# Kernel optimization log

Measured on AMD Instinct MI355X. Metric: run time of the kernel, lower is better.

## Reference

```python
import jax, jax.numpy as jnp
import numpy as np


def lstm_cell(x, h, c, Wih, Whh, b):
    # PyTorch LSTM gate order: i, f, g, o
    z = x @ Wih.T + h @ Whh.T + b
    i, f, g, o = jnp.split(z, 4, axis=-1)
    c = jax.nn.sigmoid(f) * c + jax.nn.sigmoid(i) * jnp.tanh(g)
    h = jax.nn.sigmoid(o) * jnp.tanh(c)
    return h, c


def run_dir(xs, Wih, Whh, b, reverse):
    # xs: [S, B, D_in] -> outputs [S, B, H], final (h, c)
    B = xs.shape[1]
    H = Whh.shape[1]
    init = (jnp.zeros((B, H), xs.dtype), jnp.zeros((B, H), xs.dtype))
    def step(carry, x):
        h, c = carry
        h, c = lstm_cell(x, h, c, Wih, Whh, b)
        return (h, c), h
    (h, c), ys = jax.lax.scan(step, init, xs, reverse=reverse)
    return ys, h, c


def _p(k, shape, scale=0.05):
    return jax.random.normal(k, shape, dtype=jnp.float32) * scale


def setup_inputs():
    V, E, H = 32000, 128, 256
    B, S, T = 32, 256, 64
    ks = jax.random.split(jax.random.key(0), 24)
    return {
        "src": jax.random.randint(ks[0], (B, S), 0, V),
        "tgt": jax.random.randint(ks[1], (B, T), 0, V),
        "emb": _p(ks[2], (V, E), 1.0),
        "enc_Wih_l0": _p(ks[3], (2, 4 * H, E)),
        "enc_Whh_l0": _p(ks[4], (2, 4 * H, H)),
        "enc_b_l0": _p(ks[5], (2, 4 * H)),
        "enc_Wih_l1": _p(ks[6], (2, 4 * H, 2 * H)),
        "enc_Whh_l1": _p(ks[7], (2, 4 * H, H)),
        "enc_b_l1": _p(ks[8], (2, 4 * H)),
        "dec_Wih0": _p(ks[9], (8 * H, E + 2 * H)),
        "dec_Whh0": _p(ks[10], (8 * H, 2 * H)),
        "dec_b0": _p(ks[11], (8 * H,)),
        "dec_Wih1": _p(ks[12], (8 * H, 2 * H)),
        "dec_Whh1": _p(ks[13], (8 * H, 2 * H)),
        "dec_b1": _p(ks[14], (8 * H,)),
        "attn_W1": _p(ks[15], (H, 4 * H)),
        "attn_b1": _p(ks[16], (H,)),
        "attn_W2": _p(ks[17], (1, H)),
        "attn_b2": _p(ks[18], (1,)),
        "out_W1": _p(ks[19], (H, 2 * H)),
        "out_b1": _p(ks[20], (H,)),
        "out_W2": _p(ks[21], (V, H)),
        "out_b2": _p(ks[22], (V,)),
    }


def reference(src, tgt, emb, enc_Wih_l0, enc_Whh_l0, enc_b_l0, enc_Wih_l1, enc_Whh_l1, enc_b_l1, dec_Wih0, dec_Whh0, dec_b0, dec_Wih1, dec_Whh1, dec_b1, attn_W1, attn_b1, attn_W2, attn_b2, out_W1, out_b1, out_W2, out_b2):
    # dropout layers are identity in eval mode
    H2 = dec_Whh0.shape[1]  # 2*hidden_dim = 512
    src_e = emb[src]                        # [B, S, E]
    tgt_e = emb[tgt]                        # [B, T, E]
    xs = jnp.swapaxes(src_e, 0, 1)          # [S, B, E]

    # 2-layer bidirectional encoder
    yf, hf0, cf0 = run_dir(xs, enc_Wih_l0[0], enc_Whh_l0[0], enc_b_l0[0], False)
    yb, hb0, cb0 = run_dir(xs, enc_Wih_l0[1], enc_Whh_l0[1], enc_b_l0[1], True)
    y0 = jnp.concatenate([yf, yb], axis=-1)  # [S, B, 2H]
    yf1, hf1, cf1 = run_dir(y0, enc_Wih_l1[0], enc_Whh_l1[0], enc_b_l1[0], False)
    yb1, hb1, cb1 = run_dir(y0, enc_Wih_l1[1], enc_Whh_l1[1], enc_b_l1[1], True)
    enc_out = jnp.swapaxes(jnp.concatenate([yf1, yb1], axis=-1), 0, 1)  # [B, S, 2H]

    # decoder init: per-layer concat of fwd/bwd final states (matches the view/transpose)
    h0 = jnp.concatenate([hf0, hb0], axis=-1)
    c0 = jnp.concatenate([cf0, cb0], axis=-1)
    h1 = jnp.concatenate([hf1, hb1], axis=-1)
    c1 = jnp.concatenate([cf1, cb1], axis=-1)

    # attention: Linear(4H, H) split into decoder-hidden part and encoder part
    W1_dec = attn_W1[:, :H2]
    W1_enc = attn_W1[:, H2:]
    enc_proj = jnp.einsum('bsd,hd->bsh', enc_out, W1_enc) + attn_b1  # precompute once

    dec_xs = jnp.swapaxes(tgt_e[:, :-1, :], 0, 1)  # [T-1, B, E]

    def step(carry, x_t):
        h0, c0, h1, c1 = carry
        e = jnp.tanh(enc_proj + (h1 @ W1_dec.T)[:, None, :])  # [B, S, H]
        scores = e @ attn_W2[0] + attn_b2[0]                  # [B, S]
        a = jax.nn.softmax(scores, axis=1)
        ctx = jnp.einsum('bs,bsd->bd', a, enc_out)            # [B, 2H]
        x = jnp.concatenate([x_t, ctx], axis=-1)              # [B, E+2H]
        h0, c0 = lstm_cell(x, h0, c0, dec_Wih0, dec_Whh0, dec_b0)
        h1, c1 = lstm_cell(h0, h1, c1, dec_Wih1, dec_Whh1, dec_b1)
        hid = jax.nn.relu(h1 @ out_W1.T + out_b1)
        logits = hid @ out_W2.T + out_b2                      # [B, V]
        return (h0, c0, h1, c1), logits

    _, ys = jax.lax.scan(step, (h0, c0, h1, c1), dec_xs)      # [T-1, B, V]
    return jnp.swapaxes(ys, 0, 1)                             # [B, T-1, V]
```

## Files before the change

kernel.cpp:

```cpp
#include <hip/hip_runtime.h>

#define BB_ 32
#define SS_ 256
#define TD_ 63
#define EE_ 128
#define VV_ 32000

typedef unsigned short u16;
typedef unsigned int u32;
typedef unsigned long long u64;
typedef __attribute__((ext_vector_type(8))) short short8v;
typedef __attribute__((ext_vector_type(4))) float f32x4;

__device__ __forceinline__ float sigf(float x){ return 1.0f/(1.0f+__expf(-x)); }
__device__ __forceinline__ float tanhf_fast(float x){ return 1.0f - 2.0f/(__expf(2.0f*x)+1.0f); }
__device__ __forceinline__ u16 f2bf(float f){
  unsigned u = __float_as_uint(f);
  u += 0x7fff + ((u >> 16) & 1);
  return (u16)(u >> 16);
}
__device__ __forceinline__ u32 packbf(float a, float b){
  return (u32)f2bf(a) | ((u32)f2bf(b) << 16);
}
__device__ __forceinline__ float bflo(u32 v){ return __uint_as_float(v << 16); }
__device__ __forceinline__ float bfhi(u32 v){ return __uint_as_float(v & 0xffff0000u); }

__device__ __forceinline__ u32 aldu(const u32* p){
  return __hip_atomic_load(p, __ATOMIC_RELAXED, __HIP_MEMORY_SCOPE_AGENT);
}
__device__ __forceinline__ u64 ald64u(const u32* p){
  return __hip_atomic_load((const u64*)p, __ATOMIC_RELAXED, __HIP_MEMORY_SCOPE_AGENT);
}
__device__ __forceinline__ void astu(u32* p, u32 v){
  __hip_atomic_store(p, v, __ATOMIC_RELAXED, __HIP_MEMORY_SCOPE_AGENT);
}
__device__ __forceinline__ float aldf(const float* p){
  return __hip_atomic_load(p, __ATOMIC_RELAXED, __HIP_MEMORY_SCOPE_AGENT);
}
__device__ __forceinline__ void astf(float* p, float v){
  __hip_atomic_store(p, v, __ATOMIC_RELAXED, __HIP_MEMORY_SCOPE_AGENT);
}
__device__ __forceinline__ void vdrain(){ asm volatile("s_waitcnt vmcnt(0)" ::: "memory"); }

__device__ __forceinline__ short8v mkfrag(u64 a, u64 b){
  union { u32 u[4]; short8v v; } c;
  c.u[0] = (u32)a; c.u[1] = (u32)(a >> 32);
  c.u[2] = (u32)b; c.u[3] = (u32)(b >> 32);
  return c.v;
}

__device__ __forceinline__ f32x4 mma8(const char* ldsA, int akk0, const u32* brow,
                                      int boff, int lk, int l, f32x4 acc){
  u64 bq[16];
  #pragma unroll
  for (int k2 = 0; k2 < 8; k2++){
    int a = boff + k2*16 + lk*4;
    bq[2*k2]   = ald64u(brow + a);
    bq[2*k2+1] = ald64u(brow + a + 2);
  }
  #pragma unroll
  for (int k2 = 0; k2 < 8; k2++){
    short8v aF = *(const short8v*)(ldsA + (((akk0 + k2)*64) + l)*16);
    acc = __builtin_amdgcn_mfma_f32_16x16x32_bf16(aF, mkfrag(bq[2*k2], bq[2*k2+1]), acc, 0, 0, 0);
  }
  return acc;
}

#define OFF_Z        0u
#define OFF_Y0       16777216u
#define OFF_Y1       20971520u
#define OFF_ZPRE     25165824u
#define OFF_H1ALL    29294592u
#define OFF_SRCE     30326784u
#define OFF_TGTE     31375360u
#define OFF_EPROJ    31633408u
#define OFF_ENCA0    33730560u
#define OFF_ENCA1    33992704u
#define OFF_DECA     34254848u
#define OFF_ATP      36352000u
#define OFF_E0H      36417536u
#define OFF_E0C      36433920u
#define OFF_E1H      36450304u
#define OFF_E1C      36466688u
#define OFF_H0P      36483072u
#define OFF_H1P      36499456u
#define OFF_CTXP     36515840u
#define OFF_CTXS     36532224u
#define OFF_Y1P      36532288u
#define OFF_HEXA     38629440u
#define OFF_HEXB     38645824u
#define OFF_BARS     38662208u

__device__ __forceinline__ void icbar(unsigned* ctr, unsigned target){
  vdrain();
  __syncthreads();
  if (threadIdx.x == 0){
    __hip_atomic_fetch_add(ctr, 1u, __ATOMIC_RELAXED, __HIP_MEMORY_SCOPE_AGENT);
    while (__hip_atomic_load(ctr, __ATOMIC_RELAXED, __HIP_MEMORY_SCOPE_AGENT) < target)
      __builtin_amdgcn_s_sleep(2);
  }
  __syncthreads();
  asm volatile("" ::: "memory");
}

__device__ __forceinline__ void icbar2(unsigned* base, unsigned gen){
  vdrain();
  __syncthreads();
  if (threadIdx.x == 0){
    unsigned g = blockIdx.x & 15u;
    unsigned old = __hip_atomic_fetch_add(&base[g*16], 1u, __ATOMIC_RELAXED, __HIP_MEMORY_SCOPE_AGENT);
    if ((old & 7u) == 7u)
      __hip_atomic_fetch_add(&base[256], 1u, __ATOMIC_RELAXED, __HIP_MEMORY_SCOPE_AGENT);
    while (__hip_atomic_load(&base[256], __ATOMIC_RELAXED, __HIP_MEMORY_SCOPE_AGENT) < gen*16u)
      __builtin_amdgcn_s_sleep(2);
  }
  __syncthreads();
  asm volatile("" ::: "memory");
}

__global__ void k_zero(float* __restrict__ p, int n){
  int i = blockIdx.x*256 + threadIdx.x;
  if (i < n) p[i] = 0.f;
}

__global__ void k_gather(const int* __restrict__ src, const int* __restrict__ tgt,
                         const float* __restrict__ emb,
                         float* __restrict__ src_e, float* __restrict__ tgt_e){
  int idx = blockIdx.x*256 + threadIdx.x;
  const int total = (8192 + 2016) * 32;
  if (idx >= total) return;
  int row = idx >> 5, j = idx & 31;
  int tok; float* dst;
  if (row < 8192){
    int s = row >> 5, b = row & 31;
    tok = src[b*SS_ + s];
    dst = src_e + (size_t)row*EE_;
  } else {
    int r2 = row - 8192;
    int t = r2 >> 5, b = r2 & 31;
    tok = tgt[b*64 + t];
    dst = tgt_e + (size_t)r2*EE_;
  }
  float4 v = *(const float4*)(emb + (size_t)tok*EE_ + j*4);
  *(float4*)(dst + j*4) = v;
}

__global__ void k_prep_encA(const float* __restrict__ W, u16* __restrict__ out){
  int idx = blockIdx.x*256 + threadIdx.x;
  if (idx >= 524288) return;
  int j = idx & 7, l = (idx>>3)&63, kk = (idx>>9)&7, m = (idx>>12)&7, us = (idx>>15)&7, d = (idx>>18)&1;
  int r = l & 15, g = r & 3, ut = r >> 2;
  int gcol = g*256 + us*32 + m*4 + ut;
  int k = kk*32 + (l>>4)*8 + j;
  out[idx] = f2bf(W[((size_t)d*1024 + gcol)*256 + k]);
}

__global__ void k_prep_decA(const float* __restrict__ Wih0, const float* __restrict__ Whh0,
                            const float* __restrict__ Wih1, const float* __restrict__ Whh1,
                            u16* __restrict__ out){
  int idx = blockIdx.x*256 + threadIdx.x;
  if (idx >= 4194304) return;
  int j = idx & 7, l = (idx>>3)&63, kk = (idx>>9)&31, cell = (idx>>14)&1, B = idx>>15;
  int r = l & 15;
  int ul = r >> 2, g = r & 3;
  int gcol = g*512 + B*4 + ul;
  int k = kk*32 + (l>>4)*8 + j;
  float wv;
  if (cell == 0) wv = (k < 512) ? Wih0[(size_t)gcol*640 + 128 + k] : Whh0[(size_t)gcol*512 + k - 512];
  else           wv = (k < 512) ? Wih1[(size_t)gcol*512 + k]       : Whh1[(size_t)gcol*512 + k - 512];
  out[idx] = f2bf(wv);
}

__global__ void k_prep_aTp(const float* __restrict__ aW1, u32* __restrict__ aTp){
  int idx = blockIdx.x*256 + threadIdx.x;
  if (idx >= 65536) return;
  int j2 = idx >> 8, c = idx & 255;
  aTp[idx] = packbf(aW1[(size_t)c*1024 + 2*j2], aW1[(size_t)c*1024 + 2*j2 + 1]);
}

__global__ void k_dinit(const float* __restrict__ eh0, const float* __restrict__ eh1,
                        u32* __restrict__ h0p, u32* __restrict__ h1p){
  int idx = blockIdx.x*256 + threadIdx.x;
  if (idx >= 8192) return;
  int b = idx >> 8, i = idx & 255;
  int dd = (2*i) >> 8, uu = (2*i) & 255;
  const float* p0 = eh0 + ((size_t)dd*32 + b)*256 + uu;
  const float* p1 = eh1 + ((size_t)dd*32 + b)*256 + uu;
  h0p[b*256 + i] = packbf(p0[0], p0[1]);
  h1p[b*256 + i] = packbf(p1[0], p1[1]);
}

__global__ __launch_bounds__(256) void k_mgemm(
    const float* __restrict__ A, const float* __restrict__ Bm,
    const float* __restrict__ bias, float* __restrict__ C,
    int M, int N, int K, int ldb, int boff, int flags){
  __shared__ u16 As[128*72];
  __shared__ u16 Bs[128*72];
  int tid = threadIdx.x;
  int m0 = blockIdx.x*128, n0 = blockIdx.y*128;
  int l = tid & 63, w = tid >> 6;
  int wr = w >> 1, wc = w & 1;
  int lr = l & 15, lk = (l >> 4) * 8;
  f32x4 acc[4][4];
  #pragma unroll
  for (int m=0;m<4;m++)
    #pragma unroll
    for (int n=0;n<4;n++) acc[m][n] = (f32x4){0.f,0.f,0.f,0.f};

  int r = tid >> 1, half = tid & 1;
  bool aval = (m0 + r) < M;
  const float* arow = A + (size_t)(m0 + r)*K + half*32;
  const float* brow = Bm + (size_t)(n0 + r)*ldb + boff + half*32;
  u16* asd = &As[r*72 + half*32];
  u16* bsd = &Bs[r*72 + half*32];

  for (int k0 = 0; k0 < K; k0 += 64){
    #pragma unroll
    for (int j = 0; j < 4; j++){
      float4 x = make_float4(0.f,0.f,0.f,0.f), y = x;
      if (aval){
        x = *(const float4*)(arow + k0 + j*8);
        y = *(const float4*)(arow + k0 + j*8 + 4);
      }
      asd[j*8+0]=f2bf(x.x); asd[j*8+1]=f2bf(x.y); asd[j*8+2]=f2bf(x.z); asd[j*8+3]=f2bf(x.w);
      asd[j*8+4]=f2bf(y.x); asd[j*8+5]=f2bf(y.y); asd[j*8+6]=f2bf(y.z); asd[j*8+7]=f2bf(y.w);
      float4 p = *(const float4*)(brow + k0 + j*8);
      float4 q = *(const float4*)(brow + k0 + j*8 + 4);
      bsd[j*8+0]=f2bf(p.x); bsd[j*8+1]=f2bf(p.y); bsd[j*8+2]=f2bf(p.z); bsd[j*8+3]=f2bf(p.w);
      bsd[j*8+4]=f2bf(q.x); bsd[j*8+5]=f2bf(q.y); bsd[j*8+6]=f2bf(q.z); bsd[j*8+7]=f2bf(q.w);
    }
    __syncthreads();
    #pragma unroll
    for (int kk = 0; kk < 2; kk++){
      short8v aF[4], bF[4];
      #pragma unroll
      for (int m = 0; m < 4; m++)
        aF[m] = *(short8v*)&As[(wr*64 + m*16 + lr)*72 + kk*32 + lk];
      #pragma unroll
      for (int n = 0; n < 4; n++)
        bF[n] = *(short8v*)&Bs[(wc*64 + n*16 + lr)*72 + kk*32 + lk];
      #pragma unroll
      for (int m = 0; m < 4; m++)
        #pragma unroll
        for (int n = 0; n < 4; n++)
          acc[m][n] = __builtin_amdgcn_mfma_f32_16x16x32_bf16(aF[m], bF[n], acc[m][n], 0, 0, 0);
    }
    __syncthreads();
  }

  #pragma unroll
  for (int m = 0; m < 4; m++){
    int gr0 = m0 + wr*64 + m*16 + (l >> 4)*4;
    #pragma unroll
    for (int n = 0; n < 4; n++){
      int gc = n0 + wc*64 + n*16 + (l & 15);
      float bv = bias[gc];
      #pragma unroll
      for (int j = 0; j < 4; j++){
        int gr = gr0 + j;
        if (gr >= M) continue;
        float v = acc[m][n][j] + bv;
        if (flags & 1) v = fmaxf(v, 0.f);
        if (flags & 2){
          int t = gr >> 5, b = gr & 31;
          C[((size_t)(b*63 + t))*(size_t)N + gc] = v;
        } else {
          C[(size_t)gr*N + gc] = v;
        }
      }
    }
  }
}

__global__ __launch_bounds__(256) void k_enc_scan(
    const float* __restrict__ Z, const u16* __restrict__ encA,
    float* __restrict__ y, u32* __restrict__ y1p,
    u32* __restrict__ hexp, float* __restrict__ hfin, float* __restrict__ cfin,
    unsigned* __restrict__ bars){
  extern __shared__ char smem[];
  char* ldsA = smem;
  int blk = blockIdx.x, tid = threadIdx.x;
  int us = blk & 7, bh = (blk>>3)&1, d = blk>>4;
  int dom = d*2 + bh;
  unsigned* ctr = bars + dom*16;
  int w = tid >> 6, l = tid & 63;
  int lr = l & 15, lk = l >> 4;
  { const uint4* s = (const uint4*)(encA + (size_t)(d*8+us)*32768);
    uint4* dst = (uint4*)ldsA;
    for (int i = tid; i < 4096; i += 256) dst[i] = s[i]; }
  float c0 = 0.f, c1 = 0.f;
  int b_g = bh*16 + lr;
  int uc0 = us*32 + w*8 + lk, uc1 = uc0 + 4;
  u32* hx = hexp + dom*4096;
  __syncthreads();
  for (int i = 0; i < 256; i++){
    int t = d ? (255 - i) : i;
    int par_r = (i & 1) ^ 1;
    u64 bq[16];
    const u32* bs = hx + par_r*2048 + lr*128;
    #pragma unroll
    for (int kk = 0; kk < 8; kk++){
      bq[2*kk]   = ald64u(bs + kk*16 + lk*4);
      bq[2*kk+1] = ald64u(bs + kk*16 + lk*4 + 2);
    }
    const float* zr = Z + ((size_t)t*32 + b_g)*2048 + d*1024;
    float za[4], zb[4];
    #pragma unroll
    for (int j = 0; j < 4; j++){ za[j] = zr[j*256 + uc0]; zb[j] = zr[j*256 + uc1]; }
    f32x4 acc0 = (f32x4){0.f,0.f,0.f,0.f};
    f32x4 acc1 = (f32x4){0.f,0.f,0.f,0.f};
    #pragma unroll
    for (int kk = 0; kk < 8; kk++){
      short8v bF = mkfrag(bq[2*kk], bq[2*kk+1]);
      short8v a0 = *(const short8v*)(ldsA + (((w*2+0)*8 + kk)*64 + l)*16);
      short8v a1 = *(const short8v*)(ldsA + (((w*2+1)*8 + kk)*64 + l)*16);
      acc0 = __builtin_amdgcn_mfma_f32_16x16x32_bf16(a0, bF, acc0, 0, 0, 0);
      acc1 = __builtin_amdgcn_mfma_f32_16x16x32_bf16(a1, bF, acc1, 0, 0, 0);
    }
    float z0 = acc0[0]+za[0], z1 = acc0[1]+za[1], z2 = acc0[2]+za[2], z3 = acc0[3]+za[3];
    float cn = sigf(z1)*c0 + sigf(z0)*tanhf_fast(z2);
    float hn0 = sigf(z3)*tanhf_fast(cn); c0 = cn;
    z0 = acc1[0]+zb[0]; z1 = acc1[1]+zb[1]; z2 = acc1[2]+zb[2]; z3 = acc1[3]+zb[3];
    cn = sigf(z1)*c1 + sigf(z0)*tanhf_fast(z2);
    float hn1 = sigf(z3)*tanhf_fast(cn); c1 = cn;
    size_t yr = ((size_t)t*32 + b_g)*512 + d*256;
    y[yr + uc0] = hn0; y[yr + uc1] = hn1;
    float p0 = __shfl_xor(hn0, 16);
    float p1 = __shfl_xor(hn1, 16);
    if ((lk & 1) == 0){
      int base = us*16 + w*4 + (lk >> 1);
      u32 pk0 = packbf(hn0, p0), pk1 = packbf(hn1, p1);
      astu(hx + (i&1)*2048 + lr*128 + base,     pk0);
      astu(hx + (i&1)*2048 + lr*128 + base + 2, pk1);
      if (y1p){
        int gb = d*128 + base;
        y1p[((size_t)t*32 + b_g)*256 + gb]     = pk0;
        y1p[((size_t)t*32 + b_g)*256 + gb + 2] = pk1;
      }
    }
    if (i == 255){
      size_t fb = ((size_t)d*32 + b_g)*256;
      hfin[fb + uc0] = hn0; hfin[fb + uc1] = hn1;
      cfin[fb + uc0] = c0;  cfin[fb + uc1] = c1;
      break;
    }
    icbar(ctr, (unsigned)(i+1)*8u);
  }
}

__global__ __launch_bounds__(256) void k_dec_scan(
    const u32* __restrict__ aTp, const float* __restrict__ eproj,
    const float* __restrict__ aW2, const u32* __restrict__ y1p,
    const float* __restrict__ zpre, const float* __restrict__ db1,
    const u16* __restrict__ decA,
    const float* __restrict__ e0c, const float* __restrict__ e1c,
    u32* __restrict__ h0p, u32* __restrict__ h1p,
    u32* __restrict__ ctxp, float* __restrict__ ctxS,
    float* __restrict__ H1all, unsigned* __restrict__ bars){
  extern __shared__ char smem[];
  char* ldsA = smem;
  float* h1s = (float*)(smem + 65536);
  float* qs  = h1s + 512;
  float* w2s = qs + 256;
  float* es  = w2s + 256;
  int Bid = blockIdx.x, tid = threadIdx.x;
  int w = tid >> 6, l = tid & 63;
  int n_ = w & 1, kh = w >> 1;
  int lr = l & 15, lk = l >> 4;
  { const uint4* s = (const uint4*)(decA + (size_t)Bid*32768);
    uint4* d4 = (uint4*)ldsA;
    for (int i = tid; i < 4096; i += 256) d4[i] = s[i]; }
  bool att = (Bid < 64);
  int attb = Bid >> 1, attp = Bid & 1;
  if (att) w2s[tid] = aW2[tid];
  int u = Bid*4 + lk;
  int b_e = n_*16 + lr;
  float c0r=0.f, c1r=0.f, d0=0.f, d1=0.f, d2=0.f, d3=0.f;
  if (kh == 1){
    int dd = u >> 8, uu = u & 255;
    c0r = e0c[((size_t)dd*32 + b_e)*256 + uu];
    c1r = e1c[((size_t)dd*32 + b_e)*256 + uu];
    d0 = db1[u]; d1 = db1[512+u]; d2 = db1[1024+u]; d3 = db1[1536+u];
  }
  int brow_off = (n_*16 + lr)*256;
  __syncthreads();
  unsigned gen = 0;
  for (int t = 0; t < TD_; t++){
    int hp = t & 1;
    if (att){
      int b = attb;
      u32 hv = aldu(h1p + hp*8192 + b*256 + tid);
      h1s[2*tid] = bflo(hv); h1s[2*tid+1] = bfhi(hv);
      __syncthreads();
      float q0=0.f,q1=0.f,q2=0.f,q3=0.f;
      for (int j2 = 0; j2 < 256; j2 += 4){
        u32 w0 = aTp[(j2+0)*256 + tid];
        u32 w1 = aTp[(j2+1)*256 + tid];
        u32 w2 = aTp[(j2+2)*256 + tid];
        u32 w3 = aTp[(j2+3)*256 + tid];
        q0 += bflo(w0)*h1s[2*j2]   + bfhi(w0)*h1s[2*j2+1];
        q1 += bflo(w1)*h1s[2*j2+2] + bfhi(w1)*h1s[2*j2+3];
        q2 += bflo(w2)*h1s[2*j2+4] + bfhi(w2)*h1s[2*j2+5];
        q3 += bflo(w3)*h1s[2*j2+6] + bfhi(w3)*h1s[2*j2+7];
      }
      qs[tid] = (q0+q1)+(q2+q3);
      __syncthreads();
      int sl = tid >> 3, hc = tid & 7;
      for (int so = 0; so < 4; so++){
        int s = attp*128 + so*32 + sl;
        const float4* ep = (const float4*)(eproj + ((size_t)s*32 + b)*256 + hc*32);
        const float4* q4 = (const float4*)(qs + hc*32);
        const float4* w4 = (const float4*)(w2s + hc*32);
        float acc = 0.f;
        #pragma unroll
        for (int k = 0; k < 8; k++){
          float4 e = ep[k], qq = q4[k], ww = w4[k];
          acc += tanhf_fast(e.x+qq.x)*ww.x + tanhf_fast(e.y+qq.y)*ww.y
               + tanhf_fast(e.z+qq.z)*ww.z + tanhf_fast(e.w+qq.w)*ww.w;
        }
        acc += __shfl_xor(acc, 1);
        acc += __shfl_xor(acc, 2);
        acc += __shfl_xor(acc, 4);
        if (hc == 0) es[so*32 + sl] = __expf(acc);
      }
      __syncthreads();
      float a0 = 0.f, a1 = 0.f, S = 0.f;
      size_t ybase = ((size_t)(attp*128)*32 + b)*256 + tid;
      for (int si = 0; si < 128; si++){
        float e = es[si];
        S += e;
        u32 yv = y1p[ybase + (size_t)si*8192];
        a0 += e*bflo(yv); a1 += e*bfhi(yv);
      }
      astu(ctxp + attp*8192 + b*256 + tid, packbf(a0, a1));
      if (tid == 0) astf(ctxS + attp*32 + b, S);
    }
    icbar2(bars, ++gen);
    {
      f32x4 acc = (f32x4){0.f,0.f,0.f,0.f};
      if (kh == 0){
        acc = mma8(ldsA, 0, ctxp + brow_off,        0,   lk, l, acc);
        acc = mma8(ldsA, 8, ctxp + brow_off,        128, lk, l, acc);
        acc = mma8(ldsA, 0, ctxp + 8192 + brow_off, 0,   lk, l, acc);
        acc = mma8(ldsA, 8, ctxp + 8192 + brow_off, 128, lk, l, acc);
      } else {
        acc = mma8(ldsA, 16, h0p + hp*8192 + brow_off, 0,   lk, l, acc);
        acc = mma8(ldsA, 24, h0p + hp*8192 + brow_off, 128, lk, l, acc);
      }
      float* zred = h1s;
      if (kh == 0) *(f32x4*)&zred[(n_*64 + l)*4] = acc;
      __syncthreads();
      if (kh == 1){
        f32x4 o = *(f32x4*)&zred[(n_*64 + l)*4];
        float sc = 1.0f / (aldf(ctxS + b_e) + aldf(ctxS + 32 + b_e));
        const float* zp = zpre + ((size_t)t*32 + b_e)*2048 + u;
        float z0 = o[0]*sc + acc[0] + zp[0];
        float z1 = o[1]*sc + acc[1] + zp[512];
        float z2 = o[2]*sc + acc[2] + zp[1024];
        float z3 = o[3]*sc + acc[3] + zp[1536];
        float cn = sigf(z1)*c0r + sigf(z0)*tanhf_fast(z2);
        float hn = sigf(z3)*tanhf_fast(cn);
        c0r = cn;
        float other = __shfl_xor(hn, 16);
        if ((lk & 1) == 0)
          astu(h0p + (1-hp)*8192 + b_e*256 + Bid*2 + (lk>>1), packbf(hn, other));
      }
    }
    icbar2(bars, ++gen);
    {
      f32x4 acc = (f32x4){0.f,0.f,0.f,0.f};
      if (kh == 0){
        acc = mma8(ldsA, 32, h0p + (1-hp)*8192 + brow_off, 0,   lk, l, acc);
        acc = mma8(ldsA, 40, h0p + (1-hp)*8192 + brow_off, 128, lk, l, acc);
      } else {
        acc = mma8(ldsA, 48, h1p + hp*8192 + brow_off, 0,   lk, l, acc);
        acc = mma8(ldsA, 56, h1p + hp*8192 + brow_off, 128, lk, l, acc);
      }
      float* zred = h1s;
      if (kh == 0) *(f32x4*)&zred[(n_*64 + l)*4] = acc;
      __syncthreads();
      if (kh == 1){
        f32x4 o = *(f32x4*)&zred[(n_*64 + l)*4];
        float z0 = o[0] + acc[0] + d0;
        float z1 = o[1] + acc[1] + d1;
        float z2 = o[2] + acc[2] + d2;
        float z3 = o[3] + acc[3] + d3;
        float cn = sigf(z1)*c1r + sigf(z0)*tanhf_fast(z2);
        float hn = sigf(z3)*tanhf_fast(cn);
        c1r = cn;
        H1all[((size_t)t*32 + b_e)*512 + u] = hn;
        float other = __shfl_xor(hn, 16);
        if ((lk & 1) == 0)
          astu(h1p + (1-hp)*8192 + b_e*256 + Bid*2 + (lk>>1), packbf(hn, other));
      }
    }
    if (t < TD_-1) icbar2(bars, ++gen);
  }
}

extern "C" void kernel_launch(void* const* d_in, const int* in_sizes, int n_in,
                              void* d_out, int out_size, void* d_ws, size_t ws_size,
                              hipStream_t stream){
  (void)in_sizes; (void)n_in; (void)out_size; (void)ws_size;
  const int*   src   = (const int*)d_in[0];
  const int*   tgt   = (const int*)d_in[1];
  const float* emb   = (const float*)d_in[2];
  const float* eWih0 = (const float*)d_in[3];
  const float* eWhh0 = (const float*)d_in[4];
  const float* eb0   = (const float*)d_in[5];
  const float* eWih1 = (const float*)d_in[6];
  const float* eWhh1 = (const float*)d_in[7];
  const float* eb1   = (const float*)d_in[8];
  const float* dWih0 = (const float*)d_in[9];
  const float* dWhh0 = (const float*)d_in[10];
  const float* db0   = (const float*)d_in[11];
  const float* dWih1 = (const float*)d_in[12];
  const float* dWhh1 = (const float*)d_in[13];
  const float* db1   = (const float*)d_in[14];
  const float* aW1   = (const float*)d_in[15];
  const float* ab1   = (const float*)d_in[16];
  const float* aW2   = (const float*)d_in[17];
  const float* oW1   = (const float*)d_in[19];
  const float* ob1   = (const float*)d_in[20];
  const float* oW2   = (const float*)d_in[21];
  const float* ob2   = (const float*)d_in[22];

  float* F = (float*)d_out;
  float* Z     = F + OFF_Z;
  float* y0    = F + OFF_Y0;
  float* y1    = F + OFF_Y1;
  float* zpre  = F + OFF_ZPRE;
  float* H1    = F + OFF_H1ALL;
  float* srcE  = F + OFF_SRCE;
  float* tgtE  = F + OFF_TGTE;
  float* eproj = F + OFF_EPROJ;
  u16*   encA0 = (u16*)(F + OFF_ENCA0);
  u16*   encA1 = (u16*)(F + OFF_ENCA1);
  u16*   decA  = (u16*)(F + OFF_DECA);
  u32*   aTp   = (u32*)(F + OFF_ATP);
  float* e0h   = F + OFF_E0H;
  float* e0c   = F + OFF_E0C;
  float* e1h   = F + OFF_E1H;
  float* e1c   = F + OFF_E1C;
  u32*   h0p   = (u32*)(F + OFF_H0P);
  u32*   h1p   = (u32*)(F + OFF_H1P);
  u32*   ctxp  = (u32*)(F + OFF_CTXP);
  float* ctxS  = F + OFF_CTXS;
  u32*   y1p   = (u32*)(F + OFF_Y1P);
  u32*   hexA  = (u32*)(F + OFF_HEXA);
  u32*   hexB  = (u32*)(F + OFF_HEXB);
  unsigned* bars = (unsigned*)(F + OFF_BARS);
  float* hid   = (float*)d_ws;

  hipFuncSetAttribute((const void*)k_enc_scan, hipFuncAttributeMaxDynamicSharedMemorySize, 65536);
  hipFuncSetAttribute((const void*)k_dec_scan, hipFuncAttributeMaxDynamicSharedMemorySize, 70656);

  k_zero<<<132,256,0,stream>>>(F + OFF_HEXA, 33792);
  k_gather<<<((8192+2016)*32+255)/256,256,0,stream>>>(src, tgt, emb, srcE, tgtE);
  k_prep_encA<<<2048,256,0,stream>>>(eWhh0, encA0);
  k_prep_encA<<<2048,256,0,stream>>>(eWhh1, encA1);
  k_prep_decA<<<16384,256,0,stream>>>(dWih0, dWhh0, dWih1, dWhh1, decA);
  k_prep_aTp<<<256,256,0,stream>>>(aW1, aTp);

  k_mgemm<<<dim3(64,16),256,0,stream>>>(srcE, eWih0, eb0, Z, 8192,2048,128, 128,0,0);
  k_enc_scan<<<32,256,65536,stream>>>(Z, encA0, y0, (u32*)nullptr, hexA, e0h, e0c, bars);
  k_mgemm<<<dim3(64,16),256,0,stream>>>(y0, eWih1, eb1, Z, 8192,2048,512, 512,0,0);
  k_enc_scan<<<32,256,65536,stream>>>(Z, encA1, y1, y1p, hexB, e1h, e1c, bars + 320);

  k_mgemm<<<dim3(64,2),256,0,stream>>>(y1, aW1, ab1, eproj, 8192,256,512, 1024,512,0);
  k_mgemm<<<dim3(16,16),256,0,stream>>>(tgtE, dWih0, db0, zpre, 2016,2048,128, 640,0,0);
  k_dinit<<<32,256,0,stream>>>(e0h, e1h, h0p, h1p);

  k_dec_scan<<<128,256,70656,stream>>>(aTp, eproj, aW2, y1p, zpre, db1, decA,
                                       e0c, e1c, h0p, h1p, ctxp, ctxS, H1, bars + 640);

  k_mgemm<<<dim3(16,2),256,0,stream>>>(H1, oW1, ob1, hid, 2016,256,512, 512,0,1);
  k_mgemm<<<dim3(16,250),256,0,stream>>>(hid, oW2, ob2, F, 2016,32000,256, 256,0,2);
}
```

Baseline: 4.980 ms.

## Hoist decoder recurrent matmuls before barriers and prefetch encoder gate inputs

In the decoder scan, the h0/h1 recurrent MFMA contributions for both layers are computed at the start of each step, before the attention phase and grid barrier, so they are off the post-barrier critical path. Partial sums are kept in dedicated LDS slots, which raises LDS use. The encoder scan prefetches the next step's Z gate inputs before its barrier. Other changes: eproj is stored batch-major for contiguous attention reads, the context accumulation loop is unrolled with two accumulators, and barrier spin sleep is shortened. The extra LDS and registers may reduce occupancy.

```diff
diff --git a/kernel.cpp b/kernel.cpp
--- a/kernel.cpp
+++ b/kernel.cpp
@@ -47,23 +47,6 @@
   c.u[0] = (u32)a; c.u[1] = (u32)(a >> 32);
   c.u[2] = (u32)b; c.u[3] = (u32)(b >> 32);
   return c.v;
-}
-
-__device__ __forceinline__ f32x4 mma8(const char* ldsA, int akk0, const u32* brow,
-                                      int boff, int lk, int l, f32x4 acc){
-  u64 bq[16];
-  #pragma unroll
-  for (int k2 = 0; k2 < 8; k2++){
-    int a = boff + k2*16 + lk*4;
-    bq[2*k2]   = ald64u(brow + a);
-    bq[2*k2+1] = ald64u(brow + a + 2);
-  }
-  #pragma unroll
-  for (int k2 = 0; k2 < 8; k2++){
-    short8v aF = *(const short8v*)(ldsA + (((akk0 + k2)*64) + l)*16);
-    acc = __builtin_amdgcn_mfma_f32_16x16x32_bf16(aF, mkfrag(bq[2*k2], bq[2*k2+1]), acc, 0, 0, 0);
-  }
-  return acc;
 }
 
 #define OFF_Z        0u
@@ -97,7 +80,7 @@
   if (threadIdx.x == 0){
     __hip_atomic_fetch_add(ctr, 1u, __ATOMIC_RELAXED, __HIP_MEMORY_SCOPE_AGENT);
     while (__hip_atomic_load(ctr, __ATOMIC_RELAXED, __HIP_MEMORY_SCOPE_AGENT) < target)
-      __builtin_amdgcn_s_sleep(2);
+      __builtin_amdgcn_s_sleep(1);
   }
   __syncthreads();
   asm volatile("" ::: "memory");
@@ -112,7 +95,7 @@
     if ((old & 7u) == 7u)
       __hip_atomic_fetch_add(&base[256], 1u, __ATOMIC_RELAXED, __HIP_MEMORY_SCOPE_AGENT);
     while (__hip_atomic_load(&base[256], __ATOMIC_RELAXED, __HIP_MEMORY_SCOPE_AGENT) < gen*16u)
-      __builtin_amdgcn_s_sleep(2);
+      __builtin_amdgcn_s_sleep(1);
   }
   __syncthreads();
   asm volatile("" ::: "memory");
@@ -264,6 +247,9 @@
         if (flags & 2){
           int t = gr >> 5, b = gr & 31;
           C[((size_t)(b*63 + t))*(size_t)N + gc] = v;
+        } else if (flags & 4){
+          int s = gr >> 5, b = gr & 31;
+          C[((size_t)(b*256 + s))*(size_t)N + gc] = v;
         } else {
           C[(size_t)gr*N + gc] = v;
         }
@@ -293,6 +279,13 @@
   int uc0 = us*32 + w*8 + lk, uc1 = uc0 + 4;
   u32* hx = hexp + dom*4096;
   __syncthreads();
+  float za[4], zb[4];
+  {
+    int t0 = d ? 255 : 0;
+    const float* zr = Z + ((size_t)t0*32 + b_g)*2048 + d*1024;
+    #pragma unroll
+    for (int j = 0; j < 4; j++){ za[j] = zr[j*256 + uc0]; zb[j] = zr[j*256 + uc1]; }
+  }
   for (int i = 0; i < 256; i++){
     int t = d ? (255 - i) : i;
     int par_r = (i & 1) ^ 1;
@@ -303,10 +296,6 @@
       bq[2*kk]   = ald64u(bs + kk*16 + lk*4);
       bq[2*kk+1] = ald64u(bs + kk*16 + lk*4 + 2);
     }
-    const float* zr = Z + ((size_t)t*32 + b_g)*2048 + d*1024;
-    float za[4], zb[4];
-    #pragma unroll
-    for (int j = 0; j < 4; j++){ za[j] = zr[j*256 + uc0]; zb[j] = zr[j*256 + uc1]; }
     f32x4 acc0 = (f32x4){0.f,0.f,0.f,0.f};
     f32x4 acc1 = (f32x4){0.f,0.f,0.f,0.f};
     #pragma unroll
@@ -344,6 +333,12 @@
       cfin[fb + uc0] = c0;  cfin[fb + uc1] = c1;
       break;
     }
+    {
+      int tn = d ? (254 - i) : (i + 1);
+      const float* zr = Z + ((size_t)tn*32 + b_g)*2048 + d*1024;
+      #pragma unroll
+      for (int j = 0; j < 4; j++){ za[j] = zr[j*256 + uc0]; zb[j] = zr[j*256 + uc1]; }
+    }
     icbar(ctr, (unsigned)(i+1)*8u);
   }
 }
@@ -359,7 +354,11 @@
     float* __restrict__ H1all, unsigned* __restrict__ bars){
   extern __shared__ char smem[];
   char* ldsA = smem;
-  float* h1s = (float*)(smem + 65536);
+  f32x4* pAc0 = (f32x4*)(smem + 65536);
+  f32x4* pAc1 = (f32x4*)(smem + 65536 + 2048);
+  f32x4* pB   = (f32x4*)(smem + 65536 + 4096);
+  f32x4* pC   = (f32x4*)(smem + 65536 + 6144);
+  float* h1s = (float*)(smem + 65536 + 8192);
   float* qs  = h1s + 512;
   float* w2s = qs + 256;
   float* es  = w2s + 256;
@@ -367,6 +366,7 @@
   int w = tid >> 6, l = tid & 63;
   int n_ = w & 1, kh = w >> 1;
   int lr = l & 15, lk = l >> 4;
+  int idx = n_*64 + l;
   { const uint4* s = (const uint4*)(decA + (size_t)Bid*32768);
     uint4* d4 = (uint4*)ldsA;
     for (int i = tid; i < 4096; i += 256) d4[i] = s[i]; }
@@ -387,6 +387,41 @@
   unsigned gen = 0;
   for (int t = 0; t < TD_; t++){
     int hp = t & 1;
+    f32x4 rA0, rA1;
+    float zp0=0.f, zp1=0.f, zp2=0.f, zp3=0.f;
+    {
+      if (kh == 1){
+        const float* zp = zpre + ((size_t)t*32 + b_e)*2048 + u;
+        zp0 = zp[0]; zp1 = zp[512]; zp2 = zp[1024]; zp3 = zp[1536];
+      }
+      const u32* r0 = h0p + hp*8192 + brow_off;
+      const u32* r1 = h1p + hp*8192 + brow_off;
+      u64 qa[16], qb[16];
+      #pragma unroll
+      for (int k2 = 0; k2 < 8; k2++){
+        int a = (kh*8 + k2)*16 + lk*4;
+        qa[2*k2] = ald64u(r0 + a); qa[2*k2+1] = ald64u(r0 + a + 2);
+      }
+      #pragma unroll
+      for (int k2 = 0; k2 < 8; k2++){
+        int a = (kh*8 + k2)*16 + lk*4;
+        qb[2*k2] = ald64u(r1 + a); qb[2*k2+1] = ald64u(r1 + a + 2);
+      }
+      f32x4 aA = (f32x4){0.f,0.f,0.f,0.f};
+      f32x4 aB = (f32x4){0.f,0.f,0.f,0.f};
+      #pragma unroll
+      for (int k2 = 0; k2 < 8; k2++){
+        short8v aF = *(const short8v*)(ldsA + (((16 + kh*8 + k2)*64) + l)*16);
+        aA = __builtin_amdgcn_mfma_f32_16x16x32_bf16(aF, mkfrag(qa[2*k2], qa[2*k2+1]), aA, 0, 0, 0);
+      }
+      #pragma unroll
+      for (int k2 = 0; k2 < 8; k2++){
+        short8v aF = *(const short8v*)(ldsA + (((48 + kh*8 + k2)*64) + l)*16);
+        aB = __builtin_amdgcn_mfma_f32_16x16x32_bf16(aF, mkfrag(qb[2*k2], qb[2*k2+1]), aB, 0, 0, 0);
+      }
+      if (kh == 0){ pAc0[idx] = aA; pAc1[idx] = aB; }
+      else        { rA0 = aA; rA1 = aB; }
+    }
     if (att){
       int b = attb;
       u32 hv = aldu(h1p + hp*8192 + b*256 + tid);
@@ -406,9 +441,10 @@
       qs[tid] = (q0+q1)+(q2+q3);
       __syncthreads();
       int sl = tid >> 3, hc = tid & 7;
+      #pragma unroll
       for (int so = 0; so < 4; so++){
         int s = attp*128 + so*32 + sl;
-        const float4* ep = (const float4*)(eproj + ((size_t)s*32 + b)*256 + hc*32);
+        const float4* ep = (const float4*)(eproj + ((size_t)attb*256 + s)*256 + hc*32);
         const float4* q4 = (const float4*)(qs + hc*32);
         const float4* w4 = (const float4*)(w2s + hc*32);
         float acc = 0.f;
@@ -424,40 +460,47 @@
         if (hc == 0) es[so*32 + sl] = __expf(acc);
       }
       __syncthreads();
-      float a0 = 0.f, a1 = 0.f, S = 0.f;
+      float a0 = 0.f, a1 = 0.f, b0 = 0.f, b1 = 0.f, S = 0.f;
       size_t ybase = ((size_t)(attp*128)*32 + b)*256 + tid;
-      for (int si = 0; si < 128; si++){
-        float e = es[si];
-        S += e;
-        u32 yv = y1p[ybase + (size_t)si*8192];
-        a0 += e*bflo(yv); a1 += e*bfhi(yv);
-      }
-      astu(ctxp + attp*8192 + b*256 + tid, packbf(a0, a1));
+      #pragma unroll 8
+      for (int si = 0; si < 128; si += 2){
+        float e0 = es[si], e1 = es[si+1];
+        u32 v0 = y1p[ybase + (size_t)si*8192];
+        u32 v1 = y1p[ybase + (size_t)(si+1)*8192];
+        S += e0 + e1;
+        a0 += e0*bflo(v0); a1 += e0*bfhi(v0);
+        b0 += e1*bflo(v1); b1 += e1*bfhi(v1);
+      }
+      astu(ctxp + attp*8192 + b*256 + tid, packbf(a0+b0, a1+b1));
       if (tid == 0) astf(ctxS + attp*32 + b, S);
     }
     icbar2(bars, ++gen);
     {
+      float Sa = 0.f, Sb = 0.f;
+      if (kh == 1){ Sa = aldf(ctxS + b_e); Sb = aldf(ctxS + 32 + b_e); }
+      const u32* rc = ctxp + kh*8192 + brow_off;
+      u64 qc[32];
+      #pragma unroll
+      for (int kk = 0; kk < 16; kk++){
+        int a = kk*16 + lk*4;
+        qc[2*kk] = ald64u(rc + a); qc[2*kk+1] = ald64u(rc + a + 2);
+      }
       f32x4 acc = (f32x4){0.f,0.f,0.f,0.f};
-      if (kh == 0){
-        acc = mma8(ldsA, 0, ctxp + brow_off,        0,   lk, l, acc);
-        acc = mma8(ldsA, 8, ctxp + brow_off,        128, lk, l, acc);
-        acc = mma8(ldsA, 0, ctxp + 8192 + brow_off, 0,   lk, l, acc);
-        acc = mma8(ldsA, 8, ctxp + 8192 + brow_off, 128, lk, l, acc);
-      } else {
-        acc = mma8(ldsA, 16, h0p + hp*8192 + brow_off, 0,   lk, l, acc);
-        acc = mma8(ldsA, 24, h0p + hp*8192 + brow_off, 128, lk, l, acc);
-      }
-      float* zred = h1s;
-      if (kh == 0) *(f32x4*)&zred[(n_*64 + l)*4] = acc;
+      #pragma unroll
+      for (int kk = 0; kk < 16; kk++){
+        short8v aF = *(const short8v*)(ldsA + ((kk*64) + l)*16);
+        acc = __builtin_amdgcn_mfma_f32_16x16x32_bf16(aF, mkfrag(qc[2*kk], qc[2*kk+1]), acc, 0, 0, 0);
+      }
+      if (kh == 0) pB[idx] = acc;
       __syncthreads();
       if (kh == 1){
-        f32x4 o = *(f32x4*)&zred[(n_*64 + l)*4];
-        float sc = 1.0f / (aldf(ctxS + b_e) + aldf(ctxS + 32 + b_e));
-        const float* zp = zpre + ((size_t)t*32 + b_e)*2048 + u;
-        float z0 = o[0]*sc + acc[0] + zp[0];
-        float z1 = o[1]*sc + acc[1] + zp[512];
-        float z2 = o[2]*sc + acc[2] + zp[1024];
-        float z3 = o[3]*sc + acc[3] + zp[1536];
+        f32x4 oc = pB[idx];
+        f32x4 oh = pAc0[idx];
+        float sc = 1.0f / (Sa + Sb);
+        float z0 = (acc[0]+oc[0])*sc + oh[0] + rA0[0] + zp0;
+        float z1 = (acc[1]+oc[1])*sc + oh[1] + rA0[1] + zp1;
+        float z2 = (acc[2]+oc[2])*sc + oh[2] + rA0[2] + zp2;
+        float z3 = (acc[3]+oc[3])*sc + oh[3] + rA0[3] + zp3;
         float cn = sigf(z1)*c0r + sigf(z0)*tanhf_fast(z2);
         float hn = sigf(z3)*tanhf_fast(cn);
         c0r = cn;
@@ -468,23 +511,28 @@
     }
     icbar2(bars, ++gen);
     {
+      const u32* rh = h0p + (1-hp)*8192 + brow_off;
+      u64 qd[16];
+      #pragma unroll
+      for (int k2 = 0; k2 < 8; k2++){
+        int a = (kh*8 + k2)*16 + lk*4;
+        qd[2*k2] = ald64u(rh + a); qd[2*k2+1] = ald64u(rh + a + 2);
+      }
       f32x4 acc = (f32x4){0.f,0.f,0.f,0.f};
-      if (kh == 0){
-        acc = mma8(ldsA, 32, h0p + (1-hp)*8192 + brow_off, 0,   lk, l, acc);
-        acc = mma8(ldsA, 40, h0p + (1-hp)*8192 + brow_off, 128, lk, l, acc);
-      } else {
-        acc = mma8(ldsA, 48, h1p + hp*8192 + brow_off, 0,   lk, l, acc);
-        acc = mma8(ldsA, 56, h1p + hp*8192 + brow_off, 128, lk, l, acc);
-      }
-      float* zred = h1s;
-      if (kh == 0) *(f32x4*)&zred[(n_*64 + l)*4] = acc;
+      #pragma unroll
+      for (int k2 = 0; k2 < 8; k2++){
+        short8v aF = *(const short8v*)(ldsA + (((32 + kh*8 + k2)*64) + l)*16);
+        acc = __builtin_amdgcn_mfma_f32_16x16x32_bf16(aF, mkfrag(qd[2*k2], qd[2*k2+1]), acc, 0, 0, 0);
+      }
+      if (kh == 0) pC[idx] = acc;
       __syncthreads();
       if (kh == 1){
-        f32x4 o = *(f32x4*)&zred[(n_*64 + l)*4];
-        float z0 = o[0] + acc[0] + d0;
-        float z1 = o[1] + acc[1] + d1;
-        float z2 = o[2] + acc[2] + d2;
-        float z3 = o[3] + acc[3] + d3;
+        f32x4 oc = pC[idx];
+        f32x4 oh = pAc1[idx];
+        float z0 = acc[0] + oc[0] + oh[0] + rA1[0] + d0;
+        float z1 = acc[1] + oc[1] + oh[1] + rA1[1] + d1;
+        float z2 = acc[2] + oc[2] + oh[2] + rA1[2] + d2;
+        float z3 = acc[3] + oc[3] + oh[3] + rA1[3] + d3;
         float cn = sigf(z1)*c1r + sigf(z0)*tanhf_fast(z2);
         float hn = sigf(z3)*tanhf_fast(cn);
         c1r = cn;
@@ -553,7 +601,7 @@
   float* hid   = (float*)d_ws;
 
   hipFuncSetAttribute((const void*)k_enc_scan, hipFuncAttributeMaxDynamicSharedMemorySize, 65536);
-  hipFuncSetAttribute((const void*)k_dec_scan, hipFuncAttributeMaxDynamicSharedMemorySize, 70656);
+  hipFuncSetAttribute((const void*)k_dec_scan, hipFuncAttributeMaxDynamicSharedMemorySize, 78336);
 
   k_zero<<<132,256,0,stream>>>(F + OFF_HEXA, 33792);
   k_gather<<<((8192+2016)*32+255)/256,256,0,stream>>>(src, tgt, emb, srcE, tgtE);
@@ -567,11 +615,11 @@
   k_mgemm<<<dim3(64,16),256,0,stream>>>(y0, eWih1, eb1, Z, 8192,2048,512, 512,0,0);
   k_enc_scan<<<32,256,65536,stream>>>(Z, encA1, y1, y1p, hexB, e1h, e1c, bars + 320);
 
-  k_mgemm<<<dim3(64,2),256,0,stream>>>(y1, aW1, ab1, eproj, 8192,256,512, 1024,512,0);
+  k_mgemm<<<dim3(64,2),256,0,stream>>>(y1, aW1, ab1, eproj, 8192,256,512, 1024,512,4);
   k_mgemm<<<dim3(16,16),256,0,stream>>>(tgtE, dWih0, db0, zpre, 2016,2048,128, 640,0,0);
   k_dinit<<<32,256,0,stream>>>(e0h, e1h, h0p, h1p);
 
-  k_dec_scan<<<128,256,70656,stream>>>(aTp, eproj, aW2, y1p, zpre, db1, decA,
+  k_dec_scan<<<128,256,78336,stream>>>(aTp, eproj, aW2, y1p, zpre, db1, decA,
                                        e0c, e1c, h0p, h1p, ctxp, ctxS, H1, bars + 640);
 
   k_mgemm<<<dim3(16,2),256,0,stream>>>(H1, oW1, ob1, hid, 2016,256,512, 512,0,1);
```

Measured after the change: 4.769 ms. 1.04x faster.
